# Kernel optimization log

Measured on AMD Instinct MI355X. Metric: run time of the kernel, lower is better.

Reference implementation:

```python
import jax, jax.numpy as jnp
import numpy as np

N_HEAD, D_MODEL, D_K, D_V = 16, 1024, 64, 64
B, S = 4, 2048


def setup_inputs() -> dict:
    key = jax.random.key(0)
    ks = jax.random.split(key, 11)
    s = 0.02
    return {
        "q": jax.random.normal(ks[0], (B, S, D_MODEL), jnp.float32),
        "k": jax.random.normal(ks[1], (B, S, D_MODEL), jnp.float32),
        "v": jax.random.normal(ks[2], (B, S, D_MODEL), jnp.float32),
        "Wq": jax.random.normal(ks[3], (D_MODEL, N_HEAD * D_K), jnp.float32) * s,
        "bq": jnp.zeros((N_HEAD * D_K,), jnp.float32),
        "Wk": jax.random.normal(ks[4], (D_MODEL, N_HEAD * D_K), jnp.float32) * s,
        "bk": jnp.zeros((N_HEAD * D_K,), jnp.float32),
        "Wv": jax.random.normal(ks[5], (D_MODEL, N_HEAD * D_V), jnp.float32) * s,
        "bv": jnp.zeros((N_HEAD * D_V,), jnp.float32),
        "Wo": jax.random.normal(ks[6], (N_HEAD * D_V, D_MODEL), jnp.float32) * s,
        "bo": jnp.zeros((D_MODEL,), jnp.float32),
    }


def reference(q, k, v, Wq, bq, Wk, bk, Wv, bv, Wo, bo):
    b, s, _ = q.shape
    # project and split heads: [B,S,H,Dk] -> [B,H,S,Dk]
    qh = (q @ Wq + bq).reshape(b, s, N_HEAD, D_K).transpose(0, 2, 1, 3)
    kh = (k @ Wk + bk).reshape(b, s, N_HEAD, D_K).transpose(0, 2, 1, 3)
    vh = (v @ Wv + bv).reshape(b, s, N_HEAD, D_V).transpose(0, 2, 1, 3)
    scale = 1.0 / jnp.sqrt(jnp.float32(D_K))
    scores = jnp.einsum("bhqd,bhkd->bhqk", qh, kh) * scale  # [B,H,S,S]
    atten = jax.nn.softmax(scores, axis=-1)
    out = jnp.einsum("bhqk,bhkd->bhqd", atten, vh)  # [B,H,S,Dv]
    out = out.transpose(0, 2, 1, 3).reshape(b, s, N_HEAD * D_V)
    return out @ Wo + bo
```

## Files before the change

### kernel.cpp

```cpp
#include <hip/hip_runtime.h>

typedef unsigned short u16;
typedef __attribute__((ext_vector_type(4))) float f32x4;
typedef __attribute__((ext_vector_type(16))) float f32x16;
typedef __attribute__((ext_vector_type(8))) short bf16x8;
typedef __attribute__((ext_vector_type(4))) u16 u16x4;
typedef __attribute__((ext_vector_type(8))) u16 u16x8;

#define MFMA16(a, b, c) __builtin_amdgcn_mfma_f32_16x16x32_bf16((a), (b), (c), 0, 0, 0)
#define MFMA32(a, b, c) __builtin_amdgcn_mfma_f32_32x32x16_bf16((a), (b), (c), 0, 0, 0)

__device__ __forceinline__ u16 f2bf(float f) {
  union { float f; unsigned u; } x; x.f = f;
  unsigned r = x.u + 0x7fffu + ((x.u >> 16) & 1u);
  return (u16)(r >> 16);
}

__device__ __forceinline__ unsigned cvtpk(float lo, float hi) {
  unsigned r;
  asm("v_cvt_pk_bf16_f32 %0, %1, %2" : "=v"(r) : "v"(lo), "v"(hi));
  return r;
}

__device__ __forceinline__ void gl_lds16(const void* g, void* l) {
  __builtin_amdgcn_global_load_lds((const __attribute__((address_space(1))) void*)g,
                                   (__attribute__((address_space(3))) void*)l,
                                   16, 0, 0);
}

__global__ __launch_bounds__(256) void cvtT_k(const float* __restrict__ W0, const float* __restrict__ W1,
                                              const float* __restrict__ W2, const float* __restrict__ W3,
                                              u16* __restrict__ T0, u16* __restrict__ T1,
                                              u16* __restrict__ T2, u16* __restrict__ T3) {
  __shared__ u16 t[64][72];
  const float* W; u16* T;
  switch (blockIdx.z) {
    case 0: W = W0; T = T0; break;
    case 1: W = W1; T = T1; break;
    case 2: W = W2; T = T2; break;
    default: W = W3; T = T3; break;
  }
  const int tid = threadIdx.x;
  const int tr = blockIdx.x, tc = blockIdx.y;
#pragma unroll
  for (int i = 0; i < 4; ++i) {
    int row = i * 16 + (tid >> 4);
    int c4 = tid & 15;
    float4 v = *(const float4*)&W[(size_t)(tr * 64 + row) * 1024 + tc * 64 + c4 * 4];
    t[row][c4 * 4 + 0] = f2bf(v.x);
    t[row][c4 * 4 + 1] = f2bf(v.y);
    t[row][c4 * 4 + 2] = f2bf(v.z);
    t[row][c4 * 4 + 3] = f2bf(v.w);
  }
  __syncthreads();
#pragma unroll
  for (int i = 0; i < 4; ++i) {
    int orow = i * 16 + (tid >> 4);
    int occ = tid & 15;
    u16x4 o;
#pragma unroll
    for (int j = 0; j < 4; ++j) o[j] = t[occ * 4 + j][orow];
    *(u16x4*)&T[(size_t)(tc * 64 + orow) * 1024 + tr * 64 + occ * 4] = o;
  }
}

__global__ __launch_bounds__(256) void gemm_qkv_k(const float* __restrict__ Xq, const float* __restrict__ Xk,
                                                  const float* __restrict__ Xv, const u16* __restrict__ WTb,
                                                  const float* __restrict__ bq, const float* __restrict__ bk,
                                                  const float* __restrict__ bv,
                                                  u16* __restrict__ Qh, u16* __restrict__ Kh,
                                                  u16* __restrict__ Vt, float qscale) {
  __shared__ u16 As[128 * 64];
  __shared__ u16 Bs[128 * 64];
  const int tid = threadIdx.x;
  const int lane = tid & 63;
  const int w = tid >> 6;
  const int which = blockIdx.y >> 3;
  const int m0 = blockIdx.x * 128;
  const int n0 = (blockIdx.y & 7) * 128;
  const float* X = which == 0 ? Xq : (which == 1 ? Xk : Xv);
  const u16* WT = WTb + (size_t)which * 1024 * 1024;
  const float* bias = which == 0 ? bq : (which == 1 ? bk : bv);
  const int wr = (w >> 1) * 64;
  const int wc = (w & 1) * 64;
  const int srow = lane >> 3;
  const int sch = (lane & 7) * 8;
  const int arow = tid >> 4;
  const int acol = (tid & 15) * 4;
  f32x4 acc[4][4] = {};

  for (int ks = 0; ks < 16; ++ks) {
    const int k0 = ks * 64;
#pragma unroll
    for (int i = 0; i < 4; ++i) {
      int row = i * 32 + w * 8 + srow;
      gl_lds16(WT + (size_t)(n0 + row) * 1024 + k0 + sch, &Bs[(i * 32 + w * 8) * 64]);
    }
#pragma unroll
    for (int g = 0; g < 2; ++g) {
      float4 va[4];
#pragma unroll
      for (int i = 0; i < 4; ++i) {
        int row = (g * 4 + i) * 16 + arow;
        va[i] = *(const float4*)&X[(size_t)(m0 + row) * 1024 + k0 + acol];
      }
#pragma unroll
      for (int i = 0; i < 4; ++i) {
        int row = (g * 4 + i) * 16 + arow;
        u16x4 o;
        o[0] = f2bf(va[i].x); o[1] = f2bf(va[i].y); o[2] = f2bf(va[i].z); o[3] = f2bf(va[i].w);
        *(u16x4*)&As[row * 64 + acol] = o;
      }
    }
    __syncthreads();
#pragma unroll
    for (int kk = 0; kk < 2; ++kk) {
      bf16x8 a[4], b[4];
#pragma unroll
      for (int t = 0; t < 4; ++t) {
        a[t] = *(const bf16x8*)&As[(wr + t * 16 + (lane & 15)) * 64 + kk * 32 + (lane >> 4) * 8];
        b[t] = *(const bf16x8*)&Bs[(wc + t * 16 + (lane & 15)) * 64 + kk * 32 + (lane >> 4) * 8];
      }
#pragma unroll
      for (int mi = 0; mi < 4; ++mi)
#pragma unroll
        for (int ni = 0; ni < 4; ++ni)
          acc[mi][ni] = MFMA16(a[mi], b[ni], acc[mi][ni]);
    }
    __syncthreads();
  }

  const int lr = (lane >> 4) * 4;
  const int lc = lane & 15;
  if (which <= 1) {
    u16* ob = which == 0 ? Qh : Kh;
    float scale = which == 0 ? qscale : 1.0f;
#pragma unroll
    for (int mi = 0; mi < 4; ++mi)
#pragma unroll
      for (int ni = 0; ni < 4; ++ni) {
        int n = n0 + wc + ni * 16 + lc;
        float bb = bias[n];
        int h = n >> 6, d = n & 63;
#pragma unroll
        for (int r = 0; r < 4; ++r) {
          int m = m0 + wr + mi * 16 + lr + r;
          int b = m >> 11, s = m & 2047;
          ob[(((size_t)(b * 16 + h) * 2048 + s) << 6) + d] = f2bf((acc[mi][ni][r] + bb) * scale);
        }
      }
  } else {
#pragma unroll
    for (int mi = 0; mi < 4; ++mi)
#pragma unroll
      for (int ni = 0; ni < 4; ++ni) {
        int n = n0 + wc + ni * 16 + lc;
        float bb = bias[n];
        int h = n >> 6, d = n & 63;
        int m = m0 + wr + mi * 16 + lr;
        int b = m >> 11, s = m & 2047;
        u16x4 pk;
#pragma unroll
        for (int r = 0; r < 4; ++r) pk[r] = f2bf(acc[mi][ni][r] + bb);
        *(u16x4*)&Vt[((size_t)(b * 16 + h) * 64 + d) * 2048 + s] = pk;
      }
  }
}

__global__ __launch_bounds__(256) void gemm_o_k(const u16* __restrict__ X, const u16* __restrict__ WT,
                                                const float* __restrict__ bias, float* __restrict__ out) {
  __shared__ u16 As[128 * 64];
  __shared__ u16 Bs[128 * 64];
  const int tid = threadIdx.x;
  const int lane = tid & 63;
  const int w = tid >> 6;
  const int m0 = blockIdx.x * 128;
  const int n0 = blockIdx.y * 128;
  const int wr = (w >> 1) * 64;
  const int wc = (w & 1) * 64;
  const int srow = lane >> 3;
  const int sch = (lane & 7) * 8;
  f32x4 acc[4][4] = {};

  for (int ks = 0; ks < 16; ++ks) {
    const int k0 = ks * 64;
#pragma unroll
    for (int i = 0; i < 4; ++i) {
      int row = i * 32 + w * 8 + srow;
      gl_lds16(X + (size_t)(m0 + row) * 1024 + k0 + sch, &As[(i * 32 + w * 8) * 64]);
      gl_lds16(WT + (size_t)(n0 + row) * 1024 + k0 + sch, &Bs[(i * 32 + w * 8) * 64]);
    }
    __syncthreads();
#pragma unroll
    for (int kk = 0; kk < 2; ++kk) {
      bf16x8 a[4], b[4];
#pragma unroll
      for (int t = 0; t < 4; ++t) {
        a[t] = *(const bf16x8*)&As[(wr + t * 16 + (lane & 15)) * 64 + kk * 32 + (lane >> 4) * 8];
        b[t] = *(const bf16x8*)&Bs[(wc + t * 16 + (lane & 15)) * 64 + kk * 32 + (lane >> 4) * 8];
      }
#pragma unroll
      for (int mi = 0; mi < 4; ++mi)
#pragma unroll
        for (int ni = 0; ni < 4; ++ni)
          acc[mi][ni] = MFMA16(a[mi], b[ni], acc[mi][ni]);
    }
    __syncthreads();
  }

  const int lr = (lane >> 4) * 4;
  const int lc = lane & 15;
#pragma unroll
  for (int mi = 0; mi < 4; ++mi)
#pragma unroll
    for (int ni = 0; ni < 4; ++ni) {
      int n = n0 + wc + ni * 16 + lc;
      float bb = bias[n];
#pragma unroll
      for (int r = 0; r < 4; ++r) {
        int m = m0 + wr + mi * 16 + lr + r;
        out[(size_t)m * 1024 + n] = acc[mi][ni][r] + bb;
      }
    }
}

__global__ __launch_bounds__(512) void attn_k(const u16* __restrict__ Qh, const u16* __restrict__ Kh,
                                              const u16* __restrict__ Vt, u16* __restrict__ AO) {
  __shared__ u16 SMEM[4 * 8192];
  const int lane = threadIdx.x & 63, w = threadIdx.x >> 6;
  const int hi = lane >> 5, q = lane & 31;

  const int id = blockIdx.x;
  const int bh = ((id >> 3) & 7) * 8 + (id & 7);
  const int qt = id >> 6;
  const int q0 = qt * 256 + w * 32;

  const u16* Qb = Qh + (size_t)bh * 2048 * 64;
  const u16* Kb = Kh + (size_t)bh * 2048 * 64;
  const u16* Vb = Vt + (size_t)bh * 64 * 2048;

  bf16x8 qf[4];
#pragma unroll
  for (int c = 0; c < 4; ++c)
    qf[c] = *(const bf16x8*)&Qb[(size_t)(q0 + q) * 64 + c * 16 + hi * 8];

  bf16x8 onesf;
#pragma unroll
  for (int i = 0; i < 8; ++i) onesf[i] = (short)0x3F80;

  f32x16 o0 = {}, o1 = {}, ol = {};
  const int lo8 = lane * 8;

  const int srowK = (w & 1) * 32 + q;
  const int sck = ((w >> 1) * 2 + hi) * 8;

#define STAGE(slot_, kt_) do {                                                       \
    int k0_ = (kt_) * 64;                                                            \
    gl_lds16(Kb + (size_t)(k0_ + srowK) * 64 + sck, &SMEM[(slot_) * 8192 + w * 512]);          \
    gl_lds16(Vb + (size_t)srowK * 2048 + k0_ + sck, &SMEM[(slot_) * 8192 + 4096 + w * 512]);   \
  } while (0)

  STAGE(0, 0);
  STAGE(1, 1);
  STAGE(2, 2);

  for (int kt = 0; kt < 32; ++kt) {
    if (kt < 30)       asm volatile("s_waitcnt vmcnt(4)" ::: "memory");
    else if (kt == 30) asm volatile("s_waitcnt vmcnt(2)" ::: "memory");
    else               asm volatile("s_waitcnt vmcnt(0)" ::: "memory");
    __builtin_amdgcn_s_barrier();
    if (kt <= 28) STAGE((kt + 3) & 3, kt + 3);
    __builtin_amdgcn_sched_barrier(0);

    const u16* Kc = &SMEM[(kt & 3) * 8192];
    const u16* Vc = Kc + 4096;

    f32x16 s0 = {}, s1 = {};
    __builtin_amdgcn_s_setprio(1);
#pragma unroll
    for (int c = 0; c < 4; ++c) {
      bf16x8 k0 = *(const bf16x8*)&Kc[(c * 2) * 512 + lo8];
      bf16x8 k1 = *(const bf16x8*)&Kc[(c * 2 + 1) * 512 + lo8];
      s0 = MFMA32(k0, qf[c], s0);
      s1 = MFMA32(k1, qf[c], s1);
    }
    __builtin_amdgcn_s_setprio(0);

#pragma unroll
    for (int i = 0; i < 16; ++i) {
      s0[i] = __builtin_exp2f(s0[i]);
      s1[i] = __builtin_exp2f(s1[i]);
    }

    __builtin_amdgcn_s_setprio(1);
#pragma unroll
    for (int t = 0; t < 4; ++t) {
      unsigned wA, wB, wC, wD;
      if (t == 0) { wA = cvtpk(s0[0], s0[1]); wB = cvtpk(s0[2], s0[3]); wC = cvtpk(s0[4], s0[5]); wD = cvtpk(s0[6], s0[7]); }
      else if (t == 1) { wA = cvtpk(s0[8], s0[9]); wB = cvtpk(s0[10], s0[11]); wC = cvtpk(s0[12], s0[13]); wD = cvtpk(s0[14], s0[15]); }
      else if (t == 2) { wA = cvtpk(s1[0], s1[1]); wB = cvtpk(s1[2], s1[3]); wC = cvtpk(s1[4], s1[5]); wD = cvtpk(s1[6], s1[7]); }
      else { wA = cvtpk(s1[8], s1[9]); wB = cvtpk(s1[10], s1[11]); wC = cvtpk(s1[12], s1[13]); wD = cvtpk(s1[14], s1[15]); }
      asm("v_permlane32_swap_b32 %0, %1" : "+v"(wA), "+v"(wC));
      asm("v_permlane32_swap_b32 %0, %1" : "+v"(wB), "+v"(wD));
      union { unsigned u[4]; bf16x8 v; } pf;
      pf.u[0] = wA; pf.u[1] = wB; pf.u[2] = wC; pf.u[3] = wD;
      bf16x8 v0 = *(const bf16x8*)&Vc[(t * 2) * 512 + lo8];
      bf16x8 v1 = *(const bf16x8*)&Vc[(t * 2 + 1) * 512 + lo8];
      o0 = MFMA32(v0, pf.v, o0);
      o1 = MFMA32(v1, pf.v, o1);
      ol = MFMA32(onesf, pf.v, ol);
    }
    __builtin_amdgcn_s_setprio(0);
  }
#undef STAGE

  __builtin_amdgcn_s_barrier();

  float inv = 1.0f / ol[0];
  u16* ep = SMEM + w * 2048;
#pragma unroll
  for (int g = 0; g < 2; ++g) {
    const f32x16 oo = g ? o1 : o0;
#pragma unroll
    for (int j = 0; j < 8; ++j) {
      int d = g * 32 + (j & 1) * 2 + ((j >> 1) & 1) * 8 + (j >> 2) * 16 + 4 * hi;
      unsigned pw = cvtpk(oo[2 * j] * inv, oo[2 * j + 1] * inv);
      *(unsigned*)&ep[q * 64 + ((d >> 3) ^ (q & 7)) * 8 + (d & 7)] = pw;
    }
  }
  asm volatile("s_waitcnt lgkmcnt(0)" ::: "memory");
  const int b = bh >> 4, h = bh & 15;
#pragma unroll
  for (int i = 0; i < 4; ++i) {
    int r = i * 8 + (lane >> 3), c = lane & 7;
    u16x8 vv = *(const u16x8*)&ep[r * 64 + ((c ^ (r & 7)) * 8)];
    size_t row = (size_t)b * 2048 + q0 + r;
    *(u16x8*)&AO[row * 1024 + h * 64 + c * 8] = vv;
  }
}

extern "C" void kernel_launch(void* const* d_in, const int* in_sizes, int n_in,
                              void* d_out, int out_size, void* d_ws, size_t ws_size,
                              hipStream_t stream) {
  const float* q  = (const float*)d_in[0];
  const float* k  = (const float*)d_in[1];
  const float* v  = (const float*)d_in[2];
  const float* Wq = (const float*)d_in[3];
  const float* bq = (const float*)d_in[4];
  const float* Wk = (const float*)d_in[5];
  const float* bk = (const float*)d_in[6];
  const float* Wv = (const float*)d_in[7];
  const float* bv = (const float*)d_in[8];
  const float* Wo = (const float*)d_in[9];
  const float* bo = (const float*)d_in[10];
  float* out = (float*)d_out;

  char* ws = (char*)d_ws;
  const size_t SZX = (size_t)8192 * 1024 * 2;
  const size_t SZW = (size_t)1024 * 1024 * 2;
  u16* AO  = (u16*)(ws);
  u16* WTq = (u16*)(ws + 3 * SZX);
  u16* WTk = (u16*)(ws + 3 * SZX + SZW);
  u16* WTv = (u16*)(ws + 3 * SZX + 2 * SZW);
  u16* WTo = (u16*)(ws + 3 * SZX + 3 * SZW);
  u16* Qh  = (u16*)(ws + 3 * SZX + 4 * SZW);
  u16* Kh  = (u16*)(ws + 4 * SZX + 4 * SZW);
  u16* Vt  = (u16*)(ws + 5 * SZX + 4 * SZW);

  cvtT_k<<<dim3(16, 16, 4), dim3(256), 0, stream>>>(Wq, Wk, Wv, Wo, WTq, WTk, WTv, WTo);

  gemm_qkv_k<<<dim3(64, 24), dim3(256), 0, stream>>>(q, k, v, WTq, bq, bk, bv, Qh, Kh, Vt,
                                                     0.125f * 1.4426950408889634f);

  attn_k<<<dim3(512), dim3(512), 0, stream>>>(Qh, Kh, Vt, AO);

  gemm_o_k<<<dim3(64, 8), dim3(256), 0, stream>>>(AO, WTo, bo, out);
}
```

Before: 223.5 us.

## Double-buffer QKV GEMM LDS tiles and widen blocks to 512 threads

```diff
diff --git a/kernel.cpp b/kernel.cpp
--- a/kernel.cpp
+++ b/kernel.cpp
@@ -64,14 +64,14 @@
   }
 }
 
-__global__ __launch_bounds__(256) void gemm_qkv_k(const float* __restrict__ Xq, const float* __restrict__ Xk,
+__global__ __launch_bounds__(512) void gemm_qkv_k(const float* __restrict__ Xq, const float* __restrict__ Xk,
                                                   const float* __restrict__ Xv, const u16* __restrict__ WTb,
                                                   const float* __restrict__ bq, const float* __restrict__ bk,
                                                   const float* __restrict__ bv,
                                                   u16* __restrict__ Qh, u16* __restrict__ Kh,
                                                   u16* __restrict__ Vt, float qscale) {
-  __shared__ u16 As[128 * 64];
-  __shared__ u16 Bs[128 * 64];
+  __shared__ u16 As[2][128 * 64];
+  __shared__ u16 Bs[2][128 * 64];
   const int tid = threadIdx.x;
   const int lane = tid & 63;
   const int w = tid >> 6;
@@ -81,54 +81,67 @@
   const float* X = which == 0 ? Xq : (which == 1 ? Xk : Xv);
   const u16* WT = WTb + (size_t)which * 1024 * 1024;
   const float* bias = which == 0 ? bq : (which == 1 ? bk : bv);
-  const int wr = (w >> 1) * 64;
-  const int wc = (w & 1) * 64;
+  const int wr = (w >> 2) * 64;
+  const int wc = (w & 3) * 32;
   const int srow = lane >> 3;
   const int sch = (lane & 7) * 8;
-  const int arow = tid >> 4;
-  const int acol = (tid & 15) * 4;
-  f32x4 acc[4][4] = {};
+  const int arow = tid >> 3;
+  const int acol = (tid & 7) * 8;
+  f32x4 acc[4][2] = {};
+  float4 va[4];
+
+#define BSTAGE(slot_, ks_) do {                                                             \
+    int k0_ = (ks_) * 64;                                                                   \
+    gl_lds16(WT + (size_t)(n0 + w * 16 + srow) * 1024 + k0_ + sch, &Bs[slot_][(w * 16) * 64]);     \
+    gl_lds16(WT + (size_t)(n0 + w * 16 + 8 + srow) * 1024 + k0_ + sch, &Bs[slot_][(w * 16 + 8) * 64]); \
+  } while (0)
+
+#define ALOAD(ks_) do {                                                                     \
+    int k0_ = (ks_) * 64;                                                                   \
+    va[0] = *(const float4*)&X[(size_t)(m0 + arow) * 1024 + k0_ + acol];                    \
+    va[1] = *(const float4*)&X[(size_t)(m0 + arow) * 1024 + k0_ + acol + 4];                \
+    va[2] = *(const float4*)&X[(size_t)(m0 + 64 + arow) * 1024 + k0_ + acol];               \
+    va[3] = *(const float4*)&X[(size_t)(m0 + 64 + arow) * 1024 + k0_ + acol + 4];           \
+  } while (0)
+
+  BSTAGE(0, 0);
+  ALOAD(0);
 
   for (int ks = 0; ks < 16; ++ks) {
-    const int k0 = ks * 64;
-#pragma unroll
-    for (int i = 0; i < 4; ++i) {
-      int row = i * 32 + w * 8 + srow;
-      gl_lds16(WT + (size_t)(n0 + row) * 1024 + k0 + sch, &Bs[(i * 32 + w * 8) * 64]);
-    }
-#pragma unroll
-    for (int g = 0; g < 2; ++g) {
-      float4 va[4];
-#pragma unroll
-      for (int i = 0; i < 4; ++i) {
-        int row = (g * 4 + i) * 16 + arow;
-        va[i] = *(const float4*)&X[(size_t)(m0 + row) * 1024 + k0 + acol];
-      }
-#pragma unroll
-      for (int i = 0; i < 4; ++i) {
-        int row = (g * 4 + i) * 16 + arow;
-        u16x4 o;
-        o[0] = f2bf(va[i].x); o[1] = f2bf(va[i].y); o[2] = f2bf(va[i].z); o[3] = f2bf(va[i].w);
-        *(u16x4*)&As[row * 64 + acol] = o;
-      }
-    }
-    __syncthreads();
+#pragma unroll
+    for (int i = 0; i < 2; ++i) {
+      int row = i * 64 + arow;
+      const float4 vlo = va[2 * i], vhi = va[2 * i + 1];
+      u16x8 o;
+      o[0] = f2bf(vlo.x); o[1] = f2bf(vlo.y); o[2] = f2bf(vlo.z); o[3] = f2bf(vlo.w);
+      o[4] = f2bf(vhi.x); o[5] = f2bf(vhi.y); o[6] = f2bf(vhi.z); o[7] = f2bf(vhi.w);
+      *(u16x8*)&As[ks & 1][row * 64 + acol] = o;
+    }
+    asm volatile("s_waitcnt lgkmcnt(0)" ::: "memory");
+    __builtin_amdgcn_s_barrier();
+    if (ks < 15) { BSTAGE((ks + 1) & 1, ks + 1); ALOAD(ks + 1); }
+    __builtin_amdgcn_sched_barrier(0);
+
+    const u16* Ac = As[ks & 1];
+    const u16* Bc = Bs[ks & 1];
 #pragma unroll
     for (int kk = 0; kk < 2; ++kk) {
-      bf16x8 a[4], b[4];
-#pragma unroll
-      for (int t = 0; t < 4; ++t) {
-        a[t] = *(const bf16x8*)&As[(wr + t * 16 + (lane & 15)) * 64 + kk * 32 + (lane >> 4) * 8];
-        b[t] = *(const bf16x8*)&Bs[(wc + t * 16 + (lane & 15)) * 64 + kk * 32 + (lane >> 4) * 8];
-      }
+      bf16x8 a[4], b[2];
+#pragma unroll
+      for (int t = 0; t < 4; ++t)
+        a[t] = *(const bf16x8*)&Ac[(wr + t * 16 + (lane & 15)) * 64 + kk * 32 + (lane >> 4) * 8];
+#pragma unroll
+      for (int u = 0; u < 2; ++u)
+        b[u] = *(const bf16x8*)&Bc[(wc + u * 16 + (lane & 15)) * 64 + kk * 32 + (lane >> 4) * 8];
 #pragma unroll
       for (int mi = 0; mi < 4; ++mi)
 #pragma unroll
-        for (int ni = 0; ni < 4; ++ni)
+        for (int ni = 0; ni < 2; ++ni)
           acc[mi][ni] = MFMA16(a[mi], b[ni], acc[mi][ni]);
     }
-    __syncthreads();
-  }
+  }
+#undef BSTAGE
+#undef ALOAD
 
   const int lr = (lane >> 4) * 4;
   const int lc = lane & 15;
@@ -138,7 +151,7 @@
 #pragma unroll
     for (int mi = 0; mi < 4; ++mi)
 #pragma unroll
-      for (int ni = 0; ni < 4; ++ni) {
+      for (int ni = 0; ni < 2; ++ni) {
         int n = n0 + wc + ni * 16 + lc;
         float bb = bias[n];
         int h = n >> 6, d = n & 63;
@@ -153,7 +166,7 @@
 #pragma unroll
     for (int mi = 0; mi < 4; ++mi)
 #pragma unroll
-      for (int ni = 0; ni < 4; ++ni) {
+      for (int ni = 0; ni < 2; ++ni) {
         int n = n0 + wc + ni * 16 + lc;
         float bb = bias[n];
         int h = n >> 6, d = n & 63;
@@ -369,7 +382,7 @@
 
   cvtT_k<<<dim3(16, 16, 4), dim3(256), 0, stream>>>(Wq, Wk, Wv, Wo, WTq, WTk, WTv, WTo);
 
-  gemm_qkv_k<<<dim3(64, 24), dim3(256), 0, stream>>>(q, k, v, WTq, bq, bk, bv, Qh, Kh, Vt,
+  gemm_qkv_k<<<dim3(64, 24), dim3(512), 0, stream>>>(q, k, v, WTq, bq, bk, bv, Qh, Kh, Vt,
                                                      0.125f * 1.4426950408889634f);
 
   attn_k<<<dim3(512), dim3(512), 0, stream>>>(Qh, Kh, Vt, AO);
```

Result: no change. 221.3 us (-1.0%).
